# Kernel optimization log

Hardware: AMD Instinct MI355X
Metric: run time of the kernel (lower is better)

## Reference

```python
import jax, jax.numpy as jnp
import numpy as np

V, D, H, L, RATIO, T_MAX = 1024, 512, 8, 11, 3, 1024
DH = D // H
HID = D * RATIO
NB, DB = 2048, 128  # bigram buckets / dim
EPS = 1e-6


def _rope_tables(T):
    pos = jnp.arange(T, dtype=jnp.float32)
    freqs = 1.0 / (10000.0 ** (jnp.arange(0, DH, 2, dtype=jnp.float32) / DH))
    emb = jnp.outer(pos, freqs)  # [T, DH/2]
    return jnp.cos(emb), jnp.sin(emb)


def _rmsnorm(x, w):
    return x * jax.lax.rsqrt(jnp.mean(x * x, axis=-1, keepdims=True) + EPS) * w


def setup_inputs() -> dict:
    key = jax.random.key(0)
    ks = jax.random.split(key, 10)
    B, T = 8, 1024
    s = 0.02
    return {
        "x": jax.random.randint(ks[0], (B, T), 0, V),
        "embed": jax.random.normal(ks[1], (V, D), jnp.float32) * s,
        "Wqkv": jax.random.normal(ks[2], (L, 3 * D, D), jnp.float32) * s,
        "Wproj": jax.random.normal(ks[3], (L, D, D), jnp.float32) * s,
        "n1_w": jnp.ones((L, D), jnp.float32),
        "n2_w": jnp.ones((L, D), jnp.float32),
        "Wfc1": jax.random.normal(ks[4], (L, HID, D), jnp.float32) * s,
        "Wfc2": jax.random.normal(ks[5], (L, D, HID), jnp.float32) * s,
        "norm_f_w": jnp.ones((D,), jnp.float32),
        "bg_embed": jax.random.normal(ks[6], (NB, DB), jnp.float32) * s,
        "bg_proj": jax.random.normal(ks[7], (V, DB), jnp.float32) * s,
    }


def _attn(x, Wqkv, Wproj, cos, sin, causal):
    B, T, C = x.shape
    qkv = x @ Wqkv.T  # [B,T,3D]
    q, k, v = jnp.split(qkv, 3, axis=-1)
    def heads(t):
        return t.reshape(B, T, H, DH).transpose(0, 2, 1, 3)  # [B,H,T,DH]
    q, k, v = heads(q), heads(k), heads(v)
    c = cos[None, None]  # [1,1,T,DH/2]
    s = sin[None, None]
    def rope(t):
        t1, t2 = t[..., : DH // 2], t[..., DH // 2 :]
        return jnp.concatenate([t1 * c - t2 * s, t1 * s + t2 * c], axis=-1)
    q, k = rope(q), rope(k)
    w = jnp.einsum("bhqd,bhkd->bhqk", q, k) * (DH ** -0.5)
    w = jnp.where(causal, w, -jnp.inf)
    w = jax.nn.softmax(w.astype(jnp.float32), axis=-1).astype(x.dtype)
    out = jnp.einsum("bhqk,bhkd->bhqd", w, v)
    self_w = jnp.diagonal(w, axis1=-2, axis2=-1)[..., None]  # [B,H,T,1]
    out = out - self_w * v  # XSA: subtract self-value contribution
    out = out.transpose(0, 2, 1, 3).reshape(B, T, C)
    return out @ Wproj.T


def reference(x, embed, Wqkv, Wproj, n1_w, n2_w, Wfc1, Wfc2, norm_f_w, bg_embed, bg_proj):
    B, T = x.shape
    cos, sin = _rope_tables(T_MAX)
    cos, sin = cos[:T], sin[:T]
    causal = jnp.tril(jnp.ones((T, T), dtype=bool))
    # bigram logits from previous token
    prev = jnp.concatenate([jnp.zeros((B, 1), x.dtype), x[:, :-1]], axis=1)
    bigram_logits = bg_embed[prev % NB] @ bg_proj.T  # [B,T,V]
    h = embed[x]
    for i in range(L):
        h = h + _attn(_rmsnorm(h, n1_w[i]), Wqkv[i], Wproj[i], cos, sin, causal)
        z = _rmsnorm(h, n2_w[i])
        h = h + jnp.square(jax.nn.relu(z @ Wfc1[i].T)) @ Wfc2[i].T
    h = _rmsnorm(h, norm_f_w)
    return h @ embed.T + bigram_logits
```

## Files before the change

kernel.cpp:

```cpp
#include <hip/hip_runtime.h>

#define NROW   8192
#define DMODEL 512
#define TSEQ   1024
#define LAYERS 11
#define HIDDEN 1536

typedef __bf16 bf16_t;
typedef bf16_t bf16x8 __attribute__((ext_vector_type(8)));
typedef bf16_t bf16x4 __attribute__((ext_vector_type(4)));
typedef float  f32x4  __attribute__((ext_vector_type(4)));
typedef unsigned int u32;
typedef u32 u32x4 __attribute__((ext_vector_type(4)));

#define GLD16(gp, lp) __builtin_amdgcn_global_load_lds( \
    (const __attribute__((address_space(1))) void*)(gp), \
    (__attribute__((address_space(3))) void*)(lp), 16, 0, 0)

__global__ void rope_table_k(float* __restrict__ cosT, float* __restrict__ sinT) {
    int i = blockIdx.x * blockDim.x + threadIdx.x;
    int t = i >> 5, j = i & 31;
    float freq = powf(10000.f, -(float)j * (1.f / 32.f));
    float ang = (float)t * freq;
    cosT[i] = cosf(ang);
    sinT[i] = sinf(ang);
}

__global__ void embed_gather_k(const int* __restrict__ x,
                               const float* __restrict__ embed,
                               float* __restrict__ h) {
    int n = blockIdx.x;
    int d = threadIdx.x;
    const float4* e = (const float4*)(embed + (size_t)x[n] * DMODEL);
    float4* hp = (float4*)(h + (size_t)n * DMODEL);
    hp[d] = e[d];
}

__global__ void bg_gather_k(const int* __restrict__ x,
                            const float* __restrict__ bge,
                            bf16_t* __restrict__ bgA) {
    int n = blockIdx.x;
    int t = n & (TSEQ - 1);
    int prev = (t == 0) ? 0 : x[n - 1];
    bgA[(size_t)n * 128 + threadIdx.x] = (bf16_t)bge[(size_t)prev * 128 + threadIdx.x];
}

__global__ void cvt_bf16_k(const float* __restrict__ in, bf16_t* __restrict__ out, int n8) {
    int i = blockIdx.x * blockDim.x + threadIdx.x;
    if (i >= n8) return;
    float4 a = ((const float4*)in)[2 * i];
    float4 b = ((const float4*)in)[2 * i + 1];
    bf16x8 o;
    o[0] = (bf16_t)a.x; o[1] = (bf16_t)a.y; o[2] = (bf16_t)a.z; o[3] = (bf16_t)a.w;
    o[4] = (bf16_t)b.x; o[5] = (bf16_t)b.y; o[6] = (bf16_t)b.z; o[7] = (bf16_t)b.w;
    ((bf16x8*)out)[i] = o;
}

__global__ __launch_bounds__(256) void rmsnorm_k(const float* __restrict__ in,
                                                 const float* __restrict__ w,
                                                 bf16_t* __restrict__ out) {
    int wv = threadIdx.x >> 6, lane = threadIdx.x & 63;
    int row = (blockIdx.x << 2) + wv;
    const float* rp = in + (size_t)row * DMODEL + lane * 8;
    float4 v0 = *(const float4*)(rp);
    float4 v1 = *(const float4*)(rp + 4);
    float ss = v0.x*v0.x + v0.y*v0.y + v0.z*v0.z + v0.w*v0.w
             + v1.x*v1.x + v1.y*v1.y + v1.z*v1.z + v1.w*v1.w;
#pragma unroll
    for (int off = 32; off; off >>= 1) ss += __shfl_xor(ss, off, 64);
    float sc = rsqrtf(ss * (1.f / DMODEL) + 1e-6f);
    const float* wp = w + lane * 8;
    float4 w0 = *(const float4*)(wp);
    float4 w1 = *(const float4*)(wp + 4);
    bf16x8 o;
    o[0] = (bf16_t)(v0.x * sc * w0.x); o[1] = (bf16_t)(v0.y * sc * w0.y);
    o[2] = (bf16_t)(v0.z * sc * w0.z); o[3] = (bf16_t)(v0.w * sc * w0.w);
    o[4] = (bf16_t)(v1.x * sc * w1.x); o[5] = (bf16_t)(v1.y * sc * w1.y);
    o[6] = (bf16_t)(v1.z * sc * w1.z); o[7] = (bf16_t)(v1.w * sc * w1.w);
    *(bf16x8*)(out + (size_t)row * DMODEL + lane * 8) = o;
}

template<int BM, int EPI>
__global__ __launch_bounds__(256) void gemm_mfma(const bf16_t* __restrict__ A,
                                                 const bf16_t* __restrict__ B,
                                                 float* __restrict__ Cf,
                                                 bf16_t* __restrict__ Cb,
                                                 const float* __restrict__ cosT,
                                                 const float* __restrict__ sinT,
                                                 int M, int N, int K, int nbx) {
    constexpr int MI  = BM / 32;
    constexpr int ACH = BM / 64;
    __shared__ __align__(16) bf16_t As[2][BM * 32];
    __shared__ __align__(16) bf16_t Bs[2][128 * 32];
    const int tid = threadIdx.x;
    const int w = tid >> 6, lane = tid & 63;

    const int nwg = (int)gridDim.x;
    const int bid = blockIdx.x;
    const int swz = (bid & 7) * (nwg >> 3) + (bid >> 3);
    const int bx = swz % nbx, by = swz / nbx;

    const int m0 = by * BM, n0 = bx * 128;
    const int wr = (w >> 1) * (BM / 2), wc = (w & 1) * 64;
    const int fr = lane & 15, fq = lane >> 4;

    f32x4 acc[MI][4] = {};

    auto stage = [&](int k0, int buf) {
#pragma unroll
        for (int c = 0; c < ACH; ++c) {
            int idx = c * 256 + tid;
            int row = idx >> 2, cs = idx & 3;
            GLD16(A + (size_t)(m0 + row) * K + k0 + cs * 8,
                  &As[buf][(size_t)(c * 256 + w * 64) * 8]);
        }
#pragma unroll
        for (int c = 0; c < 2; ++c) {
            int idx = c * 256 + tid;
            int row = idx >> 2, cs = idx & 3;
            GLD16(B + (size_t)(n0 + row) * K + k0 + cs * 8,
                  &Bs[buf][(size_t)(c * 256 + w * 64) * 8]);
        }
    };

    const int NK = K >> 5;
    stage(0, 0);
    for (int k = 0; k < NK; ++k) {
        const int cur = k & 1;
        if (k + 1 < NK) {
            stage((k + 1) << 5, cur ^ 1);
            if constexpr (BM == 128) asm volatile("s_waitcnt vmcnt(4)" ::: "memory");
            else                     asm volatile("s_waitcnt vmcnt(3)" ::: "memory");
        } else {
            asm volatile("s_waitcnt vmcnt(0)" ::: "memory");
        }
        __builtin_amdgcn_s_barrier();
        __builtin_amdgcn_sched_barrier(0);

        bf16x8 a[MI], b[4];
        const bf16_t* ap = &As[cur][(size_t)(wr + fr) * 32 + fq * 8];
        const bf16_t* bp = &Bs[cur][(size_t)(wc + fr) * 32 + fq * 8];
#pragma unroll
        for (int i = 0; i < MI; ++i) a[i] = *(const bf16x8*)(ap + i * 16 * 32);
#pragma unroll
        for (int j = 0; j < 4; ++j)  b[j] = *(const bf16x8*)(bp + j * 16 * 32);
#pragma unroll
        for (int i = 0; i < MI; ++i)
#pragma unroll
            for (int j = 0; j < 4; ++j)
                acc[i][j] = __builtin_amdgcn_mfma_f32_16x16x32_bf16(a[i], b[j], acc[i][j], 0, 0, 0);

        asm volatile("s_waitcnt lgkmcnt(0)" ::: "memory");
        __builtin_amdgcn_s_barrier();
        __builtin_amdgcn_sched_barrier(0);
    }

    if (EPI == 4) {
        const bool qk = (n0 + wc) < 1024;
#pragma unroll
        for (int i = 0; i < MI; ++i) {
#pragma unroll
            for (int q = 0; q < 4; ++q) {
                int row = m0 + wr + i * 16 + fq * 4 + q;
                size_t rb = (size_t)row * N + n0 + wc;
                if (qk) {
                    int t = row & (TSEQ - 1);
#pragma unroll
                    for (int j = 0; j < 2; ++j) {
                        int d = j * 16 + fr;
                        float c = cosT[t * 32 + d];
                        float s = sinT[t * 32 + d];
                        float v1 = acc[i][j][q], v2 = acc[i][j + 2][q];
                        Cb[rb + j * 16 + fr]       = (bf16_t)(v1 * c - v2 * s);
                        Cb[rb + (j + 2) * 16 + fr] = (bf16_t)(v1 * s + v2 * c);
                    }
                } else {
#pragma unroll
                    for (int j = 0; j < 4; ++j)
                        Cb[rb + j * 16 + fr] = (bf16_t)acc[i][j][q];
                }
            }
        }
        return;
    }
#pragma unroll
    for (int i = 0; i < MI; ++i) {
        int row = m0 + wr + i * 16 + fq * 4;
#pragma unroll
        for (int j = 0; j < 4; ++j) {
            int col = n0 + wc + j * 16 + fr;
#pragma unroll
            for (int q = 0; q < 4; ++q) {
                float v = acc[i][j][q];
                size_t off = (size_t)(row + q) * N + col;
                if (EPI == 0)      Cf[off] = v;
                else if (EPI == 1) Cf[off] += v;
                else if (EPI == 2) { v = fmaxf(v, 0.f); Cb[off] = (bf16_t)(v * v); }
            }
        }
    }
}

__global__ __launch_bounds__(256) void attn_mfma_k(const bf16_t* __restrict__ qkvb,
                                                   bf16_t* __restrict__ outb) {
    __shared__ __align__(16) bf16_t Ks[2][64 * 64];
    __shared__ __align__(16) bf16_t VsT[2][64 * 64];

    const int tid = threadIdx.x;
    const int w  = tid >> 6;
    const int ln = tid & 63;
    const int lr = ln & 15;
    const int lg = ln >> 4;

    int raw = blockIdx.x;
    int swz = (raw & 7) * 64 + (raw >> 3);
    const int bh = swz >> 3;
    const int b = bh >> 3, h = bh & 7;
    const int p = swz & 7;

    const bf16_t* Qg = qkvb + (size_t)b * TSEQ * 1536 + h * 64;
    const bf16_t* Kg = Qg + 512;
    const bf16_t* Vg = Qg + 1024;

    const int mk = tid >> 4;
    const int md = tid & 15;
    const int src0 = lr + 32 * (lg & 1);
    const int fsel = lg >> 1;

    const int ks_key = w * 16 + (ln >> 3) * 2;
    auto KSTAGE = [&](int t0, int buf) {
#pragma unroll
        for (int ii = 0; ii < 2; ++ii) {
            const int i = w * 2 + ii;
            int key = i * 8 + (ln >> 3);
            int dc  = (ln & 7) ^ (ln >> 3);
            GLD16(Kg + (size_t)(t0 + key) * 1536 + dc * 8, &Ks[buf][i * 512]);
        }
    };
    auto VLOAD = [&](int t0, bf16x4* rv) {
#pragma unroll
        for (int i = 0; i < 4; ++i)
            rv[i] = *(const bf16x4*)(Vg + (size_t)(t0 + mk * 4 + i) * 1536 + md * 4);
    };
    auto VWRITE = [&](const bf16x4* rv, int buf) {
#pragma unroll
        for (int j = 0; j < 4; ++j) {
            int row = md * 4 + j;
            bf16x4 wv;
            wv[0] = rv[0][j]; wv[1] = rv[1][j]; wv[2] = rv[2][j]; wv[3] = rv[3][j];
            int pe = row * 64 + (((mk >> 1) ^ (row & 7)) << 3) + (mk & 1) * 4;
            *(bf16x4*)&VsT[buf][pe] = wv;
        }
    };

    for (int pass = 0; pass < 2; ++pass) {
        const int qb   = pass ? (15 - p) : p;
        const int tq0b = qb << 6;
        const int tq0  = tq0b + w * 16;
        const int qrow = tq0 + lr;

        bf16x8 qreg[2];
        {
            const bf16_t* qp = Qg + (size_t)qrow * 1536 + lg * 8;
            qreg[0] = *(const bf16x8*)qp;
            qreg[1] = *(const bf16x8*)(qp + 32);
#pragma unroll
            for (int j = 0; j < 8; ++j) {
                qreg[0][j] = (bf16_t)((float)qreg[0][j] * 0.125f);
                qreg[1][j] = (bf16_t)((float)qreg[1][j] * 0.125f);
            }
        }

        f32x4 accO[4] = {};
        float mrun = -1e30f, pl = 0.f, esf = 0.f;

        {
            bf16x4 rv[4];
            KSTAGE(0, 0);
            VLOAD(0, rv);
            asm volatile("s_waitcnt vmcnt(0)" ::: "memory");
            VWRITE(rv, 0);
            asm volatile("s_waitcnt lgkmcnt(0)" ::: "memory");
            __builtin_amdgcn_s_barrier();
            __builtin_amdgcn_sched_barrier(0);
        }

        for (int t0 = 0; t0 <= tq0b; t0 += 64) {
            const int cur = (t0 >> 6) & 1;
            const bool more = t0 < tq0b;
            bf16x4 rv[4];
            if (more) {
                KSTAGE(t0 + 64, cur ^ 1);
                VLOAD(t0 + 64, rv);
            }

            f32x4 sq[4] = {};
#pragma unroll
            for (int kr = 0; kr < 4; ++kr) {
                int key = kr * 16 + lr;
#pragma unroll
                for (int s = 0; s < 2; ++s) {
                    int chunk = key * 8 + ((s * 4 + lg) ^ (key & 7));
                    bf16x8 kf = *(const bf16x8*)&Ks[cur][chunk * 8];
                    sq[kr] = __builtin_amdgcn_mfma_f32_16x16x32_bf16(kf, qreg[s], sq[kr], 0, 0, 0);
                }
            }

            float pv[4][4];
            float tm = -1e30f;
#pragma unroll
            for (int f = 0; f < 4; ++f)
#pragma unroll
                for (int r = 0; r < 4; ++r) {
                    int key = t0 + f * 16 + lg * 4 + r;
                    float sv = (key <= qrow) ? sq[f][r] : -1e30f;
                    pv[f][r] = sv;
                    tm = fmaxf(tm, sv);
                }
            tm = fmaxf(tm, __shfl_xor(tm, 16, 64));
            tm = fmaxf(tm, __shfl_xor(tm, 32, 64));
            float mnew = fmaxf(mrun, tm);
            float corr = __expf(mrun - mnew);
            mrun = mnew;
            float psum = 0.f, pd = 0.f;
#pragma unroll
            for (int f = 0; f < 4; ++f)
#pragma unroll
                for (int r = 0; r < 4; ++r) {
                    float e = __expf(pv[f][r] - mnew);
                    pv[f][r] = e;
                    psum += e;
                    int key = t0 + f * 16 + lg * 4 + r;
                    pd = (key == qrow) ? e : pd;
                }
            pl  = pl  * corr + psum;
            esf = esf * corr + pd;
#pragma unroll
            for (int dblk = 0; dblk < 4; ++dblk)
#pragma unroll
                for (int r = 0; r < 4; ++r) accO[dblk][r] *= corr;

            u32 plo[4], phi[4];
#pragma unroll
            for (int f = 0; f < 4; ++f) {
                bf16x4 t;
                t[0] = (bf16_t)pv[f][0]; t[1] = (bf16_t)pv[f][1];
                t[2] = (bf16_t)pv[f][2]; t[3] = (bf16_t)pv[f][3];
                uint2 pr = __builtin_bit_cast(uint2, t);
                plo[f] = pr.x; phi[f] = pr.y;
            }

#pragma unroll
            for (int s = 0; s < 2; ++s) {
                u32 a0 = (u32)__shfl((int)plo[s * 2],     src0,      64);
                u32 a1 = (u32)__shfl((int)phi[s * 2],     src0,      64);
                u32 a2 = (u32)__shfl((int)plo[s * 2],     src0 + 16, 64);
                u32 a3 = (u32)__shfl((int)phi[s * 2],     src0 + 16, 64);
                u32 c0 = (u32)__shfl((int)plo[s * 2 + 1], src0,      64);
                u32 c1 = (u32)__shfl((int)phi[s * 2 + 1], src0,      64);
                u32 c2 = (u32)__shfl((int)plo[s * 2 + 1], src0 + 16, 64);
                u32 c3 = (u32)__shfl((int)phi[s * 2 + 1], src0 + 16, 64);
                u32x4 bw;
                bw[0] = fsel ? c0 : a0;
                bw[1] = fsel ? c1 : a1;
                bw[2] = fsel ? c2 : a2;
                bw[3] = fsel ? c3 : a3;
                bf16x8 bfrag = __builtin_bit_cast(bf16x8, bw);
#pragma unroll
                for (int dblk = 0; dblk < 4; ++dblk) {
                    int row = dblk * 16 + lr;
                    int pe = row * 64 + (((s * 4 + lg) ^ (row & 7)) << 3);
                    bf16x8 av = *(const bf16x8*)&VsT[cur][pe];
                    accO[dblk] = __builtin_amdgcn_mfma_f32_16x16x32_bf16(av, bfrag, accO[dblk], 0, 0, 0);
                }
            }

            if (more) {
                asm volatile("s_waitcnt vmcnt(0)" ::: "memory");
                VWRITE(rv, cur ^ 1);
            }
            asm volatile("s_waitcnt lgkmcnt(0)" ::: "memory");
            __builtin_amdgcn_s_barrier();
            __builtin_amdgcn_sched_barrier(0);
        }

        pl  += __shfl_xor(pl, 16, 64);  pl  += __shfl_xor(pl, 32, 64);
        esf += __shfl_xor(esf, 16, 64); esf += __shfl_xor(esf, 32, 64);
        float rin = 1.0f / pl;
        const bf16_t* vqp = Vg + (size_t)qrow * 1536;
        bf16_t* op = outb + (size_t)(b * TSEQ + qrow) * DMODEL + h * 64;
#pragma unroll
        for (int dblk = 0; dblk < 4; ++dblk) {
            bf16x4 vq = *(const bf16x4*)(vqp + dblk * 16 + lg * 4);
            bf16x4 o4;
#pragma unroll
            for (int r = 0; r < 4; ++r)
                o4[r] = (bf16_t)((accO[dblk][r] - esf * (float)vq[r]) * rin);
            *(bf16x4*)(op + dblk * 16 + lg * 4) = o4;
        }
    }
}

static inline void cvt(const float* in, bf16_t* out, size_t n, hipStream_t s) {
    int n8 = (int)(n / 8);
    cvt_bf16_k<<<(n8 + 255) / 256, 256, 0, s>>>(in, out, n8);
}

extern "C" void kernel_launch(void* const* d_in, const int* in_sizes, int n_in,
                              void* d_out, int out_size, void* d_ws, size_t ws_size,
                              hipStream_t stream) {
    const int*   x     = (const int*)d_in[0];
    const float* embed = (const float*)d_in[1];
    const float* Wqkv  = (const float*)d_in[2];
    const float* Wproj = (const float*)d_in[3];
    const float* n1w   = (const float*)d_in[4];
    const float* n2w   = (const float*)d_in[5];
    const float* Wfc1  = (const float*)d_in[6];
    const float* Wfc2  = (const float*)d_in[7];
    const float* normf = (const float*)d_in[8];
    const float* bge   = (const float*)d_in[9];
    const float* bgp   = (const float*)d_in[10];
    float* out = (float*)d_out;

    float* ws   = (float*)d_ws;
    float* cosT = ws;
    float* sinT = cosT + 32768;
    float* h    = sinT + 32768;
    bf16_t* qkvb = (bf16_t*)(h + (size_t)NROW * DMODEL);
    bf16_t* ub   = qkvb;
    bf16_t* xn   = qkvb + (size_t)NROW * 1536;
    bf16_t* atb  = xn  + (size_t)NROW * DMODEL;
    bf16_t* bga  = atb + (size_t)NROW * DMODEL;
    bf16_t* wqb  = bga + (size_t)NROW * 128;
    bf16_t* wpb  = wqb + (size_t)LAYERS * 3 * DMODEL * DMODEL;
    bf16_t* w1b  = wpb + (size_t)LAYERS * DMODEL * DMODEL;
    bf16_t* w2b  = w1b + (size_t)LAYERS * HIDDEN * DMODEL;
    bf16_t* embb = w2b + (size_t)LAYERS * DMODEL * HIDDEN;
    bf16_t* bgpb = embb + (size_t)1024 * DMODEL;

    rope_table_k<<<128, 256, 0, stream>>>(cosT, sinT);
    embed_gather_k<<<NROW, 128, 0, stream>>>(x, embed, h);
    bg_gather_k<<<NROW, 128, 0, stream>>>(x, bge, bga);

    cvt(Wqkv,  wqb,  (size_t)LAYERS * 3 * DMODEL * DMODEL, stream);
    cvt(Wproj, wpb,  (size_t)LAYERS * DMODEL * DMODEL, stream);
    cvt(Wfc1,  w1b,  (size_t)LAYERS * HIDDEN * DMODEL, stream);
    cvt(Wfc2,  w2b,  (size_t)LAYERS * DMODEL * HIDDEN, stream);
    cvt(embed, embb, (size_t)1024 * DMODEL, stream);
    cvt(bgp,   bgpb, (size_t)1024 * 128, stream);

    for (int i = 0; i < LAYERS; ++i) {
        rmsnorm_k<<<NROW / 4, 256, 0, stream>>>(h, n1w + i * DMODEL, xn);
        gemm_mfma<128, 4><<<768, 256, 0, stream>>>(
            xn, wqb + (size_t)i * 3 * DMODEL * DMODEL, nullptr, qkvb,
            cosT, sinT, NROW, 3 * DMODEL, DMODEL, 12);
        attn_mfma_k<<<512, 256, 0, stream>>>(qkvb, atb);
        gemm_mfma<64, 1><<<512, 256, 0, stream>>>(
            atb, wpb + (size_t)i * DMODEL * DMODEL, h, nullptr,
            nullptr, nullptr, NROW, DMODEL, DMODEL, 4);
        rmsnorm_k<<<NROW / 4, 256, 0, stream>>>(h, n2w + i * DMODEL, xn);
        gemm_mfma<128, 2><<<768, 256, 0, stream>>>(
            xn, w1b + (size_t)i * HIDDEN * DMODEL, nullptr, ub,
            nullptr, nullptr, NROW, HIDDEN, DMODEL, 12);
        gemm_mfma<64, 1><<<512, 256, 0, stream>>>(
            ub, w2b + (size_t)i * DMODEL * HIDDEN, h, nullptr,
            nullptr, nullptr, NROW, DMODEL, HIDDEN, 4);
    }

    rmsnorm_k<<<NROW / 4, 256, 0, stream>>>(h, normf, xn);
    gemm_mfma<64, 0><<<1024, 256, 0, stream>>>(
        xn, embb, out, nullptr, nullptr, nullptr, NROW, 1024, DMODEL, 8);
    gemm_mfma<64, 1><<<1024, 256, 0, stream>>>(
        bga, bgpb, out, nullptr, nullptr, nullptr, NROW, 1024, 128, 8);
}
```

Measured before the change: 1.668 ms.

## Triple-buffer GEMM, split attention per query block, lazy rescale, fuse final logits GEMMs

Measured after the change: 1.592 ms. 1.05x faster.

```diff
diff --git a/kernel.cpp b/kernel.cpp
--- a/kernel.cpp
+++ b/kernel.cpp
@@ -38,11 +38,11 @@
 
 __global__ void bg_gather_k(const int* __restrict__ x,
                             const float* __restrict__ bge,
-                            bf16_t* __restrict__ bgA) {
+                            bf16_t* __restrict__ Afu) {
     int n = blockIdx.x;
     int t = n & (TSEQ - 1);
     int prev = (t == 0) ? 0 : x[n - 1];
-    bgA[(size_t)n * 128 + threadIdx.x] = (bf16_t)bge[(size_t)prev * 128 + threadIdx.x];
+    Afu[(size_t)n * 640 + 512 + threadIdx.x] = (bf16_t)bge[(size_t)prev * 128 + threadIdx.x];
 }
 
 __global__ void cvt_bf16_k(const float* __restrict__ in, bf16_t* __restrict__ out, int n8) {
@@ -56,9 +56,25 @@
     ((bf16x8*)out)[i] = o;
 }
 
+__global__ void cvt_pad_k(const float* __restrict__ in, bf16_t* __restrict__ out,
+                          int n8, int lshift, int mask, int colOff) {
+    int i = blockIdx.x * blockDim.x + threadIdx.x;
+    if (i >= n8) return;
+    int i8 = i * 8;
+    int row = i8 >> lshift;
+    int col = i8 & mask;
+    float4 a = ((const float4*)in)[2 * i];
+    float4 b = ((const float4*)in)[2 * i + 1];
+    bf16x8 o;
+    o[0] = (bf16_t)a.x; o[1] = (bf16_t)a.y; o[2] = (bf16_t)a.z; o[3] = (bf16_t)a.w;
+    o[4] = (bf16_t)b.x; o[5] = (bf16_t)b.y; o[6] = (bf16_t)b.z; o[7] = (bf16_t)b.w;
+    *(bf16x8*)&out[(size_t)row * 640 + colOff + col] = o;
+}
+
 __global__ __launch_bounds__(256) void rmsnorm_k(const float* __restrict__ in,
                                                  const float* __restrict__ w,
-                                                 bf16_t* __restrict__ out) {
+                                                 bf16_t* __restrict__ out,
+                                                 int ostride) {
     int wv = threadIdx.x >> 6, lane = threadIdx.x & 63;
     int row = (blockIdx.x << 2) + wv;
     const float* rp = in + (size_t)row * DMODEL + lane * 8;
@@ -77,7 +93,7 @@
     o[2] = (bf16_t)(v0.z * sc * w0.z); o[3] = (bf16_t)(v0.w * sc * w0.w);
     o[4] = (bf16_t)(v1.x * sc * w1.x); o[5] = (bf16_t)(v1.y * sc * w1.y);
     o[6] = (bf16_t)(v1.z * sc * w1.z); o[7] = (bf16_t)(v1.w * sc * w1.w);
-    *(bf16x8*)(out + (size_t)row * DMODEL + lane * 8) = o;
+    *(bf16x8*)(out + (size_t)row * ostride + lane * 8) = o;
 }
 
 template<int BM, int EPI>
@@ -90,8 +106,8 @@
                                                  int M, int N, int K, int nbx) {
     constexpr int MI  = BM / 32;
     constexpr int ACH = BM / 64;
-    __shared__ __align__(16) bf16_t As[2][BM * 32];
-    __shared__ __align__(16) bf16_t Bs[2][128 * 32];
+    __shared__ __align__(16) bf16_t As[3][BM * 32];
+    __shared__ __align__(16) bf16_t Bs[3][128 * 32];
     const int tid = threadIdx.x;
     const int w = tid >> 6, lane = tid & 63;
 
@@ -125,10 +141,14 @@
 
     const int NK = K >> 5;
     stage(0, 0);
+    stage(32, 1);
     for (int k = 0; k < NK; ++k) {
-        const int cur = k & 1;
-        if (k + 1 < NK) {
-            stage((k + 1) << 5, cur ^ 1);
+        const int cur = k % 3;
+        if (k + 2 < NK) {
+            stage((k + 2) << 5, (k + 2) % 3);
+            if constexpr (BM == 128) asm volatile("s_waitcnt vmcnt(8)" ::: "memory");
+            else                     asm volatile("s_waitcnt vmcnt(6)" ::: "memory");
+        } else if (k + 1 < NK) {
             if constexpr (BM == 128) asm volatile("s_waitcnt vmcnt(4)" ::: "memory");
             else                     asm volatile("s_waitcnt vmcnt(3)" ::: "memory");
         } else {
@@ -204,7 +224,7 @@
 __global__ __launch_bounds__(256) void attn_mfma_k(const bf16_t* __restrict__ qkvb,
                                                    bf16_t* __restrict__ outb) {
     __shared__ __align__(16) bf16_t Ks[2][64 * 64];
-    __shared__ __align__(16) bf16_t VsT[2][64 * 64];
+    __shared__ __align__(16) bf16_t VsT[2][2 * 64 * 32];
 
     const int tid = threadIdx.x;
     const int w  = tid >> 6;
@@ -212,11 +232,13 @@
     const int lr = ln & 15;
     const int lg = ln >> 4;
 
-    int raw = blockIdx.x;
-    int swz = (raw & 7) * 64 + (raw >> 3);
-    const int bh = swz >> 3;
+    const int bid = blockIdx.x;
+    const int qb = 15 - (bid >> 6);
+    const int bh = bid & 63;
     const int b = bh >> 3, h = bh & 7;
-    const int p = swz & 7;
+    const int tq0b = qb << 6;
+    const int tq0  = tq0b + w * 16;
+    const int qrow = tq0 + lr;
 
     const bf16_t* Qg = qkvb + (size_t)b * TSEQ * 1536 + h * 64;
     const bf16_t* Kg = Qg + 512;
@@ -226,8 +248,8 @@
     const int md = tid & 15;
     const int src0 = lr + 32 * (lg & 1);
     const int fsel = lg >> 1;
-
-    const int ks_key = w * 16 + (ln >> 3) * 2;
+    const int gofs = 8 * (lg ^ ((lr >> 2) & 3));
+
     auto KSTAGE = [&](int t0, int buf) {
 #pragma unroll
         for (int ii = 0; ii < 2; ++ii) {
@@ -243,161 +265,161 @@
             rv[i] = *(const bf16x4*)(Vg + (size_t)(t0 + mk * 4 + i) * 1536 + md * 4);
     };
     auto VWRITE = [&](const bf16x4* rv, int buf) {
+        const int s = mk >> 3;
 #pragma unroll
         for (int j = 0; j < 4; ++j) {
             int row = md * 4 + j;
             bf16x4 wv;
             wv[0] = rv[0][j]; wv[1] = rv[1][j]; wv[2] = rv[2][j]; wv[3] = rv[3][j];
-            int pe = row * 64 + (((mk >> 1) ^ (row & 7)) << 3) + (mk & 1) * 4;
-            *(bf16x4*)&VsT[buf][pe] = wv;
+            int g = (mk & 7) ^ ((md & 3) << 1);
+            *(bf16x4*)&VsT[buf][s * 2048 + row * 32 + g * 4] = wv;
         }
     };
 
-    for (int pass = 0; pass < 2; ++pass) {
-        const int qb   = pass ? (15 - p) : p;
-        const int tq0b = qb << 6;
-        const int tq0  = tq0b + w * 16;
-        const int qrow = tq0 + lr;
-
-        bf16x8 qreg[2];
-        {
-            const bf16_t* qp = Qg + (size_t)qrow * 1536 + lg * 8;
-            qreg[0] = *(const bf16x8*)qp;
-            qreg[1] = *(const bf16x8*)(qp + 32);
-#pragma unroll
-            for (int j = 0; j < 8; ++j) {
-                qreg[0][j] = (bf16_t)((float)qreg[0][j] * 0.125f);
-                qreg[1][j] = (bf16_t)((float)qreg[1][j] * 0.125f);
-            }
-        }
-
-        f32x4 accO[4] = {};
-        float mrun = -1e30f, pl = 0.f, esf = 0.f;
-
-        {
-            bf16x4 rv[4];
-            KSTAGE(0, 0);
-            VLOAD(0, rv);
+    bf16x8 qreg[2];
+    {
+        const bf16_t* qp = Qg + (size_t)qrow * 1536 + lg * 8;
+        qreg[0] = *(const bf16x8*)qp;
+        qreg[1] = *(const bf16x8*)(qp + 32);
+#pragma unroll
+        for (int j = 0; j < 8; ++j) {
+            qreg[0][j] = (bf16_t)((float)qreg[0][j] * 0.125f);
+            qreg[1][j] = (bf16_t)((float)qreg[1][j] * 0.125f);
+        }
+    }
+
+    f32x4 accO[4] = {};
+    float mrun = -1e30f, pl = 0.f, esf = 0.f;
+
+    {
+        bf16x4 rv[4];
+        KSTAGE(0, 0);
+        VLOAD(0, rv);
+        asm volatile("s_waitcnt vmcnt(0)" ::: "memory");
+        VWRITE(rv, 0);
+        asm volatile("s_waitcnt lgkmcnt(0)" ::: "memory");
+        __builtin_amdgcn_s_barrier();
+        __builtin_amdgcn_sched_barrier(0);
+    }
+
+    for (int t0 = 0; t0 <= tq0b; t0 += 64) {
+        const int cur = (t0 >> 6) & 1;
+        const bool more = t0 < tq0b;
+        bf16x4 rv[4];
+        if (more) {
+            KSTAGE(t0 + 64, cur ^ 1);
+            VLOAD(t0 + 64, rv);
+        }
+
+        f32x4 sq[4] = {};
+#pragma unroll
+        for (int kr = 0; kr < 4; ++kr) {
+            int key = kr * 16 + lr;
+#pragma unroll
+            for (int s = 0; s < 2; ++s) {
+                int chunk = key * 8 + ((s * 4 + lg) ^ (key & 7));
+                bf16x8 kf = *(const bf16x8*)&Ks[cur][chunk * 8];
+                sq[kr] = __builtin_amdgcn_mfma_f32_16x16x32_bf16(kf, qreg[s], sq[kr], 0, 0, 0);
+            }
+        }
+
+        float pv[4][4];
+        float tm = -1e30f;
+#pragma unroll
+        for (int f = 0; f < 4; ++f)
+#pragma unroll
+            for (int r = 0; r < 4; ++r) {
+                int key = t0 + f * 16 + lg * 4 + r;
+                float sv = (key <= qrow) ? sq[f][r] : -1e30f;
+                pv[f][r] = sv;
+                tm = fmaxf(tm, sv);
+            }
+        tm = fmaxf(tm, __shfl_xor(tm, 16, 64));
+        tm = fmaxf(tm, __shfl_xor(tm, 32, 64));
+
+        const bool resc = __any(tm > mrun + 8.f);
+        float mnew = resc ? fmaxf(mrun, tm) : mrun;
+        float psum = 0.f, pd = 0.f;
+        float e16[4][4];
+#pragma unroll
+        for (int f = 0; f < 4; ++f)
+#pragma unroll
+            for (int r = 0; r < 4; ++r) {
+                float e = __expf(pv[f][r] - mnew);
+                e16[f][r] = e;
+                psum += e;
+                int key = t0 + f * 16 + lg * 4 + r;
+                pd = (key == qrow) ? e : pd;
+            }
+        if (resc) {
+            float corr = __expf(mrun - mnew);
+            mrun = mnew;
+            pl  = pl  * corr + psum;
+            esf = esf * corr + pd;
+#pragma unroll
+            for (int dblk = 0; dblk < 4; ++dblk)
+#pragma unroll
+                for (int r = 0; r < 4; ++r) accO[dblk][r] *= corr;
+        } else {
+            pl  += psum;
+            esf += pd;
+        }
+
+        u32 plo[4], phi[4];
+#pragma unroll
+        for (int f = 0; f < 4; ++f) {
+            bf16x4 t;
+            t[0] = (bf16_t)e16[f][0]; t[1] = (bf16_t)e16[f][1];
+            t[2] = (bf16_t)e16[f][2]; t[3] = (bf16_t)e16[f][3];
+            uint2 pr = __builtin_bit_cast(uint2, t);
+            plo[f] = pr.x; phi[f] = pr.y;
+        }
+
+#pragma unroll
+        for (int s = 0; s < 2; ++s) {
+            u32 a0 = (u32)__shfl((int)plo[s * 2],     src0,      64);
+            u32 a1 = (u32)__shfl((int)phi[s * 2],     src0,      64);
+            u32 a2 = (u32)__shfl((int)plo[s * 2],     src0 + 16, 64);
+            u32 a3 = (u32)__shfl((int)phi[s * 2],     src0 + 16, 64);
+            u32 c0 = (u32)__shfl((int)plo[s * 2 + 1], src0,      64);
+            u32 c1 = (u32)__shfl((int)phi[s * 2 + 1], src0,      64);
+            u32 c2 = (u32)__shfl((int)plo[s * 2 + 1], src0 + 16, 64);
+            u32 c3 = (u32)__shfl((int)phi[s * 2 + 1], src0 + 16, 64);
+            u32x4 bw;
+            bw[0] = fsel ? c0 : a0;
+            bw[1] = fsel ? c1 : a1;
+            bw[2] = fsel ? c2 : a2;
+            bw[3] = fsel ? c3 : a3;
+            bf16x8 bfrag = __builtin_bit_cast(bf16x8, bw);
+#pragma unroll
+            for (int dblk = 0; dblk < 4; ++dblk) {
+                bf16x8 av = *(const bf16x8*)&VsT[cur][s * 2048 + (dblk * 16 + lr) * 32 + gofs];
+                accO[dblk] = __builtin_amdgcn_mfma_f32_16x16x32_bf16(av, bfrag, accO[dblk], 0, 0, 0);
+            }
+        }
+
+        if (more) {
             asm volatile("s_waitcnt vmcnt(0)" ::: "memory");
-            VWRITE(rv, 0);
+            VWRITE(rv, cur ^ 1);
             asm volatile("s_waitcnt lgkmcnt(0)" ::: "memory");
             __builtin_amdgcn_s_barrier();
             __builtin_amdgcn_sched_barrier(0);
         }
-
-        for (int t0 = 0; t0 <= tq0b; t0 += 64) {
-            const int cur = (t0 >> 6) & 1;
-            const bool more = t0 < tq0b;
-            bf16x4 rv[4];
-            if (more) {
-                KSTAGE(t0 + 64, cur ^ 1);
-                VLOAD(t0 + 64, rv);
-            }
-
-            f32x4 sq[4] = {};
-#pragma unroll
-            for (int kr = 0; kr < 4; ++kr) {
-                int key = kr * 16 + lr;
-#pragma unroll
-                for (int s = 0; s < 2; ++s) {
-                    int chunk = key * 8 + ((s * 4 + lg) ^ (key & 7));
-                    bf16x8 kf = *(const bf16x8*)&Ks[cur][chunk * 8];
-                    sq[kr] = __builtin_amdgcn_mfma_f32_16x16x32_bf16(kf, qreg[s], sq[kr], 0, 0, 0);
-                }
-            }
-
-            float pv[4][4];
-            float tm = -1e30f;
-#pragma unroll
-            for (int f = 0; f < 4; ++f)
-#pragma unroll
-                for (int r = 0; r < 4; ++r) {
-                    int key = t0 + f * 16 + lg * 4 + r;
-                    float sv = (key <= qrow) ? sq[f][r] : -1e30f;
-                    pv[f][r] = sv;
-                    tm = fmaxf(tm, sv);
-                }
-            tm = fmaxf(tm, __shfl_xor(tm, 16, 64));
-            tm = fmaxf(tm, __shfl_xor(tm, 32, 64));
-            float mnew = fmaxf(mrun, tm);
-            float corr = __expf(mrun - mnew);
-            mrun = mnew;
-            float psum = 0.f, pd = 0.f;
-#pragma unroll
-            for (int f = 0; f < 4; ++f)
-#pragma unroll
-                for (int r = 0; r < 4; ++r) {
-                    float e = __expf(pv[f][r] - mnew);
-                    pv[f][r] = e;
-                    psum += e;
-                    int key = t0 + f * 16 + lg * 4 + r;
-                    pd = (key == qrow) ? e : pd;
-                }
-            pl  = pl  * corr + psum;
-            esf = esf * corr + pd;
-#pragma unroll
-            for (int dblk = 0; dblk < 4; ++dblk)
-#pragma unroll
-                for (int r = 0; r < 4; ++r) accO[dblk][r] *= corr;
-
-            u32 plo[4], phi[4];
-#pragma unroll
-            for (int f = 0; f < 4; ++f) {
-                bf16x4 t;
-                t[0] = (bf16_t)pv[f][0]; t[1] = (bf16_t)pv[f][1];
-                t[2] = (bf16_t)pv[f][2]; t[3] = (bf16_t)pv[f][3];
-                uint2 pr = __builtin_bit_cast(uint2, t);
-                plo[f] = pr.x; phi[f] = pr.y;
-            }
-
-#pragma unroll
-            for (int s = 0; s < 2; ++s) {
-                u32 a0 = (u32)__shfl((int)plo[s * 2],     src0,      64);
-                u32 a1 = (u32)__shfl((int)phi[s * 2],     src0,      64);
-                u32 a2 = (u32)__shfl((int)plo[s * 2],     src0 + 16, 64);
-                u32 a3 = (u32)__shfl((int)phi[s * 2],     src0 + 16, 64);
-                u32 c0 = (u32)__shfl((int)plo[s * 2 + 1], src0,      64);
-                u32 c1 = (u32)__shfl((int)phi[s * 2 + 1], src0,      64);
-                u32 c2 = (u32)__shfl((int)plo[s * 2 + 1], src0 + 16, 64);
-                u32 c3 = (u32)__shfl((int)phi[s * 2 + 1], src0 + 16, 64);
-                u32x4 bw;
-                bw[0] = fsel ? c0 : a0;
-                bw[1] = fsel ? c1 : a1;
-                bw[2] = fsel ? c2 : a2;
-                bw[3] = fsel ? c3 : a3;
-                bf16x8 bfrag = __builtin_bit_cast(bf16x8, bw);
-#pragma unroll
-                for (int dblk = 0; dblk < 4; ++dblk) {
-                    int row = dblk * 16 + lr;
-                    int pe = row * 64 + (((s * 4 + lg) ^ (row & 7)) << 3);
-                    bf16x8 av = *(const bf16x8*)&VsT[cur][pe];
-                    accO[dblk] = __builtin_amdgcn_mfma_f32_16x16x32_bf16(av, bfrag, accO[dblk], 0, 0, 0);
-                }
-            }
-
-            if (more) {
-                asm volatile("s_waitcnt vmcnt(0)" ::: "memory");
-                VWRITE(rv, cur ^ 1);
-            }
-            asm volatile("s_waitcnt lgkmcnt(0)" ::: "memory");
-            __builtin_amdgcn_s_barrier();
-            __builtin_amdgcn_sched_barrier(0);
-        }
-
-        pl  += __shfl_xor(pl, 16, 64);  pl  += __shfl_xor(pl, 32, 64);
-        esf += __shfl_xor(esf, 16, 64); esf += __shfl_xor(esf, 32, 64);
-        float rin = 1.0f / pl;
-        const bf16_t* vqp = Vg + (size_t)qrow * 1536;
-        bf16_t* op = outb + (size_t)(b * TSEQ + qrow) * DMODEL + h * 64;
-#pragma unroll
-        for (int dblk = 0; dblk < 4; ++dblk) {
-            bf16x4 vq = *(const bf16x4*)(vqp + dblk * 16 + lg * 4);
-            bf16x4 o4;
-#pragma unroll
-            for (int r = 0; r < 4; ++r)
-                o4[r] = (bf16_t)((accO[dblk][r] - esf * (float)vq[r]) * rin);
-            *(bf16x4*)(op + dblk * 16 + lg * 4) = o4;
-        }
+    }
+
+    pl  += __shfl_xor(pl, 16, 64);  pl  += __shfl_xor(pl, 32, 64);
+    esf += __shfl_xor(esf, 16, 64); esf += __shfl_xor(esf, 32, 64);
+    float rin = 1.0f / pl;
+    const bf16_t* vqp = Vg + (size_t)qrow * 1536;
+    bf16_t* op = outb + (size_t)(b * TSEQ + qrow) * DMODEL + h * 64;
+#pragma unroll
+    for (int dblk = 0; dblk < 4; ++dblk) {
+        bf16x4 vq = *(const bf16x4*)(vqp + dblk * 16 + lg * 4);
+        bf16x4 o4;
+#pragma unroll
+        for (int r = 0; r < 4; ++r)
+            o4[r] = (bf16_t)((accO[dblk][r] - esf * (float)vq[r]) * rin);
+        *(bf16x4*)(op + dblk * 16 + lg * 4) = o4;
     }
 }
 
@@ -428,37 +450,35 @@
     float* h    = sinT + 32768;
     bf16_t* qkvb = (bf16_t*)(h + (size_t)NROW * DMODEL);
     bf16_t* ub   = qkvb;
+    bf16_t* Afu  = qkvb;
     bf16_t* xn   = qkvb + (size_t)NROW * 1536;
     bf16_t* atb  = xn  + (size_t)NROW * DMODEL;
-    bf16_t* bga  = atb + (size_t)NROW * DMODEL;
-    bf16_t* wqb  = bga + (size_t)NROW * 128;
+    bf16_t* wqb  = atb + (size_t)NROW * DMODEL;
     bf16_t* wpb  = wqb + (size_t)LAYERS * 3 * DMODEL * DMODEL;
     bf16_t* w1b  = wpb + (size_t)LAYERS * DMODEL * DMODEL;
     bf16_t* w2b  = w1b + (size_t)LAYERS * HIDDEN * DMODEL;
-    bf16_t* embb = w2b + (size_t)LAYERS * DMODEL * HIDDEN;
-    bf16_t* bgpb = embb + (size_t)1024 * DMODEL;
+    bf16_t* bfu  = w2b + (size_t)LAYERS * DMODEL * HIDDEN;
 
     rope_table_k<<<128, 256, 0, stream>>>(cosT, sinT);
     embed_gather_k<<<NROW, 128, 0, stream>>>(x, embed, h);
-    bg_gather_k<<<NROW, 128, 0, stream>>>(x, bge, bga);
 
     cvt(Wqkv,  wqb,  (size_t)LAYERS * 3 * DMODEL * DMODEL, stream);
     cvt(Wproj, wpb,  (size_t)LAYERS * DMODEL * DMODEL, stream);
     cvt(Wfc1,  w1b,  (size_t)LAYERS * HIDDEN * DMODEL, stream);
     cvt(Wfc2,  w2b,  (size_t)LAYERS * DMODEL * HIDDEN, stream);
-    cvt(embed, embb, (size_t)1024 * DMODEL, stream);
-    cvt(bgp,   bgpb, (size_t)1024 * 128, stream);
+    cvt_pad_k<<<(65536 + 255) / 256, 256, 0, stream>>>(embed, bfu, 65536, 9, 511, 0);
+    cvt_pad_k<<<(16384 + 255) / 256, 256, 0, stream>>>(bgp,   bfu, 16384, 7, 127, 512);
 
     for (int i = 0; i < LAYERS; ++i) {
-        rmsnorm_k<<<NROW / 4, 256, 0, stream>>>(h, n1w + i * DMODEL, xn);
+        rmsnorm_k<<<NROW / 4, 256, 0, stream>>>(h, n1w + i * DMODEL, xn, DMODEL);
         gemm_mfma<128, 4><<<768, 256, 0, stream>>>(
             xn, wqb + (size_t)i * 3 * DMODEL * DMODEL, nullptr, qkvb,
             cosT, sinT, NROW, 3 * DMODEL, DMODEL, 12);
-        attn_mfma_k<<<512, 256, 0, stream>>>(qkvb, atb);
+        attn_mfma_k<<<1024, 256, 0, stream>>>(qkvb, atb);
         gemm_mfma<64, 1><<<512, 256, 0, stream>>>(
             atb, wpb + (size_t)i * DMODEL * DMODEL, h, nullptr,
             nullptr, nullptr, NROW, DMODEL, DMODEL, 4);
-        rmsnorm_k<<<NROW / 4, 256, 0, stream>>>(h, n2w + i * DMODEL, xn);
+        rmsnorm_k<<<NROW / 4, 256, 0, stream>>>(h, n2w + i * DMODEL, xn, DMODEL);
         gemm_mfma<128, 2><<<768, 256, 0, stream>>>(
             xn, w1b + (size_t)i * HIDDEN * DMODEL, nullptr, ub,
             nullptr, nullptr, NROW, HIDDEN, DMODEL, 12);
@@ -467,9 +487,8 @@
             nullptr, nullptr, NROW, DMODEL, HIDDEN, 4);
     }
 
-    rmsnorm_k<<<NROW / 4, 256, 0, stream>>>(h, normf, xn);
+    rmsnorm_k<<<NROW / 4, 256, 0, stream>>>(h, normf, Afu, 640);
+    bg_gather_k<<<NROW, 128, 0, stream>>>(x, bge, Afu);
     gemm_mfma<64, 0><<<1024, 256, 0, stream>>>(
-        xn, embb, out, nullptr, nullptr, nullptr, NROW, 1024, DMODEL, 8);
-    gemm_mfma<64, 1><<<1024, 256, 0, stream>>>(
-        bga, bgpb, out, nullptr, nullptr, nullptr, NROW, 1024, 128, 8);
-}
+        Afu, bfu, out, nullptr, nullptr, nullptr, NROW, 1024, 640, 8);
+}
```
